# Performance work log

Measured on AMD Instinct MI355X. Metric: run time of the kernel, lower is better.

The kernel has to match this reference:

```python
import jax, jax.numpy as jnp
import numpy as np

TOP_K = 2


def setup_inputs() -> dict:
    key = jax.random.key(0)
    k1, k2, k3, k4, k5 = jax.random.split(key, 5)
    B, S, D, E, F = 2, 1024, 2048, 8, 768
    scale_in = 1.0 / np.sqrt(D)
    scale_ff = 1.0 / np.sqrt(F)
    return {
        "x": jax.random.normal(k1, (B, S, D), dtype=jnp.float32),
        "w_gate_router": jax.random.normal(k2, (E, D), dtype=jnp.float32) * scale_in,
        "w_gate_proj": jax.random.normal(k3, (E, F, D), dtype=jnp.float32) * scale_in,
        "w_up_proj": jax.random.normal(k4, (E, F, D), dtype=jnp.float32) * scale_in,
        "w_down_proj": jax.random.normal(k5, (E, D, F), dtype=jnp.float32) * scale_ff,
    }


def moe_forward(x, w_gate_router, w_gate_proj, w_up_proj, w_down_proj):
    E = w_gate_router.shape[0]
    # Router: scores [B,S,E], top-k selection, softmax over the k selected scores.
    scores = jnp.einsum("bsd,ed->bse", x, w_gate_router)
    topk_scores, topk_idx = jax.lax.top_k(scores, TOP_K)          # [B,S,K]
    topk_probs = jax.nn.softmax(topk_scores, axis=-1)             # [B,S,K]
    # Dense combine weights: zero for unselected experts (== scatter of topk_probs).
    weights = jnp.sum(topk_probs[..., None] * jax.nn.one_hot(topk_idx, E, dtype=x.dtype), axis=-2)  # [B,S,E]
    # Per-expert SwiGLU computed densely over all tokens (same math as
    # gather/dispatch-per-expert followed by scatter-add combine).
    gate = jnp.einsum("bsd,efd->bsef", x, w_gate_proj)            # [B,S,E,F]
    up = jnp.einsum("bsd,efd->bsef", x, w_up_proj)
    hidden = jax.nn.silu(gate) * up                                # [B,S,E,F]
    # Weighted combine: sum_e weights[b,s,e] * (hidden @ w_down[e].T)
    out = jnp.einsum("bsef,edf,bse->bsd", hidden, w_down_proj, weights)
    return out


def reference(x, w_gate_router, w_gate_proj, w_up_proj, w_down_proj):
    return moe_forward(x, w_gate_router, w_gate_proj, w_up_proj, w_down_proj)
```

## Files before the change

### kernel.cpp

```cpp
#include <hip/hip_runtime.h>

#define T_TOK 2048
#define DIM   2048
#define NEXP  8
#define FF    768
#define NGRP  16
#define BK    64

typedef unsigned short u16;
typedef unsigned int   u32;
typedef __bf16 bf16x8 __attribute__((ext_vector_type(8)));
typedef float  f32x4  __attribute__((ext_vector_type(4)));
typedef u16    u16x4  __attribute__((ext_vector_type(4)));
typedef u16    u16x8  __attribute__((ext_vector_type(8)));

#define AS1 __attribute__((address_space(1)))
#define AS3 __attribute__((address_space(3)))

__device__ __forceinline__ u16 f2bf(float f) {
    union { u32 i; float f; } v; v.f = f;
    u32 r = v.i + 0x7FFF + ((v.i >> 16) & 1);
    return (u16)(r >> 16);
}
__device__ __forceinline__ float bf2f(u16 u) {
    union { u32 i; float f; } v; v.i = ((u32)u) << 16; return v.f;
}

__device__ __forceinline__ void gload16(const u16* g, u16* l) {
    __builtin_amdgcn_global_load_lds((const AS1 u32*)g, (AS3 u32*)l, 16, 0, 0);
}

__global__ void cvt3_kernel(const float* __restrict__ s0, u16* __restrict__ d0,
                            const float* __restrict__ s1, u16* __restrict__ d1,
                            const float* __restrict__ s2, u16* __restrict__ d2) {
    const float* __restrict__ s; u16* __restrict__ d;
    switch (blockIdx.y) {
        case 0: s = s0; d = d0; break;
        case 1: s = s1; d = d1; break;
        default: s = s2; d = d2; break;
    }
    const size_t st = 1536u * 256u;
    size_t t = (size_t)blockIdx.x * 256 + threadIdx.x;
#pragma unroll
    for (int it = 0; it < 4; it++) {
        size_t i = t + (size_t)it * st;
        f32x4 a = ((const f32x4*)s)[i * 2];
        f32x4 b = ((const f32x4*)s)[i * 2 + 1];
        u16x8 o;
#pragma unroll
        for (int j = 0; j < 4; j++) { o[j] = f2bf(a[j]); o[4 + j] = f2bf(b[j]); }
        ((u16x8*)d)[i] = o;
    }
}

__global__ void router_kernel(const float* __restrict__ x, const float* __restrict__ wr,
                              int* cnt, int* rt_e, float* rt_p, u16* __restrict__ xb) {
    int wave = threadIdx.x >> 6, lane = threadIdx.x & 63;
    int t = blockIdx.x * 4 + wave;
    float xv[32];
#pragma unroll
    for (int i = 0; i < 32; i++) xv[i] = x[(size_t)t * DIM + i * 64 + lane];
#pragma unroll
    for (int i = 0; i < 32; i++) xb[(size_t)t * DIM + i * 64 + lane] = f2bf(xv[i]);
    float s[NEXP];
#pragma unroll
    for (int e = 0; e < NEXP; e++) {
        float acc = 0.f;
#pragma unroll
        for (int i = 0; i < 32; i++) acc += xv[i] * wr[(size_t)e * DIM + i * 64 + lane];
        for (int off = 32; off; off >>= 1) acc += __shfl_xor(acc, off);
        s[e] = acc;
    }
    if (lane == 0) {
        int bi = 0; float bv = s[0];
        for (int e = 1; e < NEXP; e++) if (s[e] > bv) { bv = s[e]; bi = e; }
        float sv = -1e30f; int si = 0;
        for (int e = 0; e < NEXP; e++) { if (e == bi) continue; if (s[e] > sv) { sv = s[e]; si = e; } }
        float p0 = 1.f / (1.f + __expf(sv - bv));
        float p1 = 1.f - p0;
        rt_e[t * 2 + 0] = bi; rt_e[t * 2 + 1] = si;
        rt_p[t * 2 + 0] = p0; rt_p[t * 2 + 1] = p1;
        atomicAdd(&cnt[bi * 2 + 0], 1);
        atomicAdd(&cnt[si * 2 + 1], 1);
    }
}

__global__ void scanassign_kernel(const int* cnt, const int* rt_e, const float* rt_p,
                                  int* base_g, int* tile_g, int* tile_m0, int* ntiles,
                                  int* rowtok, float* rowprob) {
    __shared__ int s_base[NGRP];
    __shared__ int s_pos[NGRP];
    int tid = threadIdx.x;
    if (tid < NGRP) s_pos[tid] = 0;
    if (tid < 64) {
        int lane = tid;
        int c = (lane < NGRP) ? cnt[lane] : 0;
        int nt_g = (c + 127) >> 7;
        int pre = 0, tpre = 0;
        for (int i = 0; i < NGRP; i++) {
            int ci = __shfl(c, i), ti = __shfl(nt_g, i);
            if (i < lane) { pre += ci; tpre += ti; }
        }
        if (lane < NGRP) {
            s_base[lane] = pre; base_g[lane] = pre;
            for (int j = 0; j < nt_g; j++) { tile_g[tpre + j] = lane; tile_m0[tpre + j] = j * 128; }
            if (lane == NGRP - 1) *ntiles = tpre + nt_g;
        }
    }
    __syncthreads();
    for (int t = tid; t < T_TOK; t += 256) {
#pragma unroll
        for (int k = 0; k < 2; k++) {
            int g = rt_e[t * 2 + k] * 2 + k;
            int pos = atomicAdd(&s_pos[g], 1);
            int row = s_base[g] + pos;
            rowtok[row] = t;
            rowprob[row] = rt_p[t * 2 + k];
        }
    }
}

__launch_bounds__(256)
__global__ void gateup_kernel(const u16* __restrict__ xb, const u16* __restrict__ wgb,
                              const u16* __restrict__ wub,
                              const int* cnt, const int* base, const int* tile_g,
                              const int* tile_m0, const int* ntiles,
                              const int* rowtok, const float* rowprob,
                              u16* __restrict__ hidden) {
    int tile = blockIdx.x;
    if (tile >= *ntiles) return;
    int g = tile_g[tile], m0 = tile_m0[tile];
    int e = g >> 1;
    int f0 = blockIdx.y * 64;
    int cg = cnt[g], bg_ = base[g];

    __shared__ u16 As[2][128 * BK];
    __shared__ u16 Bs[2][128 * BK];
    __shared__ int   tks[128];
    __shared__ float ps[128];

    int tid = threadIdx.x;
    if (tid < 128) {
        int valid = (m0 + tid) < cg;
        tks[tid] = valid ? rowtok[bg_ + m0 + tid] : 0;
        ps[tid]  = valid ? rowprob[bg_ + m0 + tid] : 0.f;
    }
    __syncthreads();

    int wave = tid >> 6, lane = tid & 63;
    int quad = lane >> 4, l16 = lane & 15;
    int wr = wave >> 1, wc = wave & 1;

    int r8  = lane >> 3;
    int csw = ((lane & 7) ^ r8) * 8;

    const u16* gA[4]; int lA[4];
#pragma unroll
    for (int gi = 0; gi < 4; gi++) {
        int row = wave * 32 + gi * 8 + r8;
        gA[gi] = xb + (size_t)tks[row] * DIM + csw;
        lA[gi] = (wave * 32 + gi * 8) * BK;
    }
    const u16* bsrc = (wave >> 1) ? wub : wgb;
    int fo = (wave & 1) * 8 + r8;
    const u16* gB[4]; int lB[4];
#pragma unroll
    for (int gi = 0; gi < 4; gi++) {
        gB[gi] = bsrc + ((size_t)e * FF + f0 + gi * 16 + fo) * DIM + csw;
        lB[gi] = (gi * 32 + wave * 8) * BK;
    }

    f32x4 acc[4][4] = {};

#pragma unroll
    for (int gi = 0; gi < 4; gi++) gload16(gA[gi], &As[0][0] + lA[gi]);
#pragma unroll
    for (int gi = 0; gi < 4; gi++) gload16(gB[gi], &Bs[0][0] + lB[gi]);

    int sw0 = ((0 * 4 + quad) ^ (l16 & 7)) * 8;
    int sw1 = ((1 * 4 + quad) ^ (l16 & 7)) * 8;

    for (int kt = 0; kt < DIM / BK; kt++) {
        int cur = kt & 1;
        int kk = (kt + 1) * BK;
        if (kk < DIM) {
#pragma unroll
            for (int gi = 0; gi < 4; gi++) gload16(gA[gi] + kk, &As[cur ^ 1][0] + lA[gi]);
#pragma unroll
            for (int gi = 0; gi < 4; gi++) gload16(gB[gi] + kk, &Bs[cur ^ 1][0] + lB[gi]);
            __builtin_amdgcn_sched_barrier(0);
            asm volatile("s_waitcnt vmcnt(8)" ::: "memory");
        } else {
            __builtin_amdgcn_sched_barrier(0);
            asm volatile("s_waitcnt vmcnt(0)" ::: "memory");
        }
        __builtin_amdgcn_s_barrier();
        __builtin_amdgcn_sched_barrier(0);
#pragma unroll
        for (int ks = 0; ks < 2; ks++) {
            int sw = ks ? sw1 : sw0;
            bf16x8 a[4], b[4];
#pragma unroll
            for (int mi = 0; mi < 4; mi++)
                a[mi] = *(const bf16x8*)&As[cur][(wr * 64 + mi * 16 + l16) * BK + sw];
#pragma unroll
            for (int ni = 0; ni < 4; ni++)
                b[ni] = *(const bf16x8*)&Bs[cur][(wc * 64 + ni * 16 + l16) * BK + sw];
#pragma unroll
            for (int mi = 0; mi < 4; mi++)
#pragma unroll
                for (int ni = 0; ni < 4; ni++)
                    acc[mi][ni] = __builtin_amdgcn_mfma_f32_16x16x32_bf16(a[mi], b[ni], acc[mi][ni], 0, 0, 0);
        }
        __builtin_amdgcn_sched_barrier(0);
        asm volatile("s_waitcnt lgkmcnt(0)" ::: "memory");
        __builtin_amdgcn_s_barrier();
    }

    int fb = f0 + wc * 32 + l16;
#pragma unroll
    for (int mi = 0; mi < 4; mi++) {
#pragma unroll
        for (int r = 0; r < 4; r++) {
            int m = wr * 64 + mi * 16 + quad * 4 + r;
            if (m0 + m < cg) {
                float p = ps[m];
                float g0 = acc[mi][0][r], u0 = acc[mi][1][r];
                float g1 = acc[mi][2][r], u1 = acc[mi][3][r];
                size_t rowo = (size_t)(bg_ + m0 + m) * FF;
                hidden[rowo + fb]      = f2bf((g0 / (1.f + __expf(-g0))) * u0 * p);
                hidden[rowo + fb + 16] = f2bf((g1 / (1.f + __expf(-g1))) * u1 * p);
            }
        }
    }
}

__launch_bounds__(256)
__global__ void down_kernel(const u16* __restrict__ hid, const u16* __restrict__ wdb,
                            const int* cnt, const int* base, const int* tile_g,
                            const int* tile_m0, const int* ntiles, const int* rowtok,
                            u16* __restrict__ out0, u16* __restrict__ out1) {
    int tile = blockIdx.x;
    if (tile >= *ntiles) return;
    int g = tile_g[tile], m0 = tile_m0[tile];
    int e = g >> 1, slot = g & 1;
    int d0 = blockIdx.y * 128;
    int cg = cnt[g], bg_ = base[g];

    __shared__ u16 As[2][128 * BK];
    __shared__ u16 Bs[2][128 * BK];
    __shared__ int tks[128];

    int tid = threadIdx.x;
    if (tid < 128) tks[tid] = ((m0 + tid) < cg) ? rowtok[bg_ + m0 + tid] : 0;
    __syncthreads();

    int wave = tid >> 6, lane = tid & 63;
    int quad = lane >> 4, l16 = lane & 15;
    int wr = wave >> 1, wc = wave & 1;

    int r8  = lane >> 3;
    int csw = ((lane & 7) ^ r8) * 8;

    const u16* gA[4]; int lA[4];
#pragma unroll
    for (int gi = 0; gi < 4; gi++) {
        int row = wave * 32 + gi * 8 + r8;
        gA[gi] = hid + (size_t)(bg_ + m0 + row) * FF + csw;
        lA[gi] = (wave * 32 + gi * 8) * BK;
    }
    const u16* gB[4]; int lB[4];
#pragma unroll
    for (int gi = 0; gi < 4; gi++) {
        int n = gi * 32 + wave * 8 + r8;
        gB[gi] = wdb + ((size_t)e * DIM + d0 + n) * FF + csw;
        lB[gi] = (gi * 32 + wave * 8) * BK;
    }

    f32x4 acc[4][4] = {};

#pragma unroll
    for (int gi = 0; gi < 4; gi++) gload16(gA[gi], &As[0][0] + lA[gi]);
#pragma unroll
    for (int gi = 0; gi < 4; gi++) gload16(gB[gi], &Bs[0][0] + lB[gi]);

    int sw0 = ((0 * 4 + quad) ^ (l16 & 7)) * 8;
    int sw1 = ((1 * 4 + quad) ^ (l16 & 7)) * 8;

    for (int kt = 0; kt < FF / BK; kt++) {
        int cur = kt & 1;
        int kk = (kt + 1) * BK;
        if (kk < FF) {
#pragma unroll
            for (int gi = 0; gi < 4; gi++) gload16(gA[gi] + kk, &As[cur ^ 1][0] + lA[gi]);
#pragma unroll
            for (int gi = 0; gi < 4; gi++) gload16(gB[gi] + kk, &Bs[cur ^ 1][0] + lB[gi]);
            __builtin_amdgcn_sched_barrier(0);
            asm volatile("s_waitcnt vmcnt(8)" ::: "memory");
        } else {
            __builtin_amdgcn_sched_barrier(0);
            asm volatile("s_waitcnt vmcnt(0)" ::: "memory");
        }
        __builtin_amdgcn_s_barrier();
        __builtin_amdgcn_sched_barrier(0);
#pragma unroll
        for (int ks = 0; ks < 2; ks++) {
            int sw = ks ? sw1 : sw0;
            bf16x8 a[4], b[4];
#pragma unroll
            for (int mi = 0; mi < 4; mi++)
                a[mi] = *(const bf16x8*)&As[cur][(wr * 64 + mi * 16 + l16) * BK + sw];
#pragma unroll
            for (int ni = 0; ni < 4; ni++)
                b[ni] = *(const bf16x8*)&Bs[cur][(wc * 64 + ni * 16 + l16) * BK + sw];
#pragma unroll
            for (int mi = 0; mi < 4; mi++)
#pragma unroll
                for (int ni = 0; ni < 4; ni++)
                    acc[mi][ni] = __builtin_amdgcn_mfma_f32_16x16x32_bf16(a[mi], b[ni], acc[mi][ni], 0, 0, 0);
        }
        __builtin_amdgcn_sched_barrier(0);
        asm volatile("s_waitcnt lgkmcnt(0)" ::: "memory");
        __builtin_amdgcn_s_barrier();
    }

    u16* outp = slot ? out1 : out0;
#pragma unroll
    for (int mi = 0; mi < 4; mi++) {
#pragma unroll
        for (int ni = 0; ni < 4; ni++) {
            int d = d0 + wc * 64 + ni * 16 + l16;
#pragma unroll
            for (int r = 0; r < 4; r++) {
                int m = wr * 64 + mi * 16 + quad * 4 + r;
                if (m0 + m < cg) {
                    outp[(size_t)tks[m] * DIM + d] = f2bf(acc[mi][ni][r]);
                }
            }
        }
    }
}

__global__ void combine_kernel(const u16* __restrict__ o0, const u16* __restrict__ o1,
                               float* __restrict__ out) {
    int i = blockIdx.x * blockDim.x + threadIdx.x;
    u16x8 a = *(const u16x8*)(o0 + (size_t)i * 8);
    u16x8 b = *(const u16x8*)(o1 + (size_t)i * 8);
    f32x4 r0, r1;
#pragma unroll
    for (int j = 0; j < 4; j++) {
        r0[j] = bf2f(a[j]) + bf2f(b[j]);
        r1[j] = bf2f(a[4 + j]) + bf2f(b[4 + j]);
    }
    *(f32x4*)(out + (size_t)i * 8) = r0;
    *(f32x4*)(out + (size_t)i * 8 + 4) = r1;
}

extern "C" void kernel_launch(void* const* d_in, const int* in_sizes, int n_in,
                              void* d_out, int out_size, void* d_ws, size_t ws_size,
                              hipStream_t stream) {
    const float* x  = (const float*)d_in[0];
    const float* wr = (const float*)d_in[1];
    const float* wg = (const float*)d_in[2];
    const float* wu = (const float*)d_in[3];
    const float* wd = (const float*)d_in[4];
    float* out = (float*)d_out;

    char* W = (char*)d_ws;
    int*   cnt     = (int*)(W + 0);
    int*   base    = (int*)(W + 128);
    int*   ntiles  = (int*)(W + 192);
    int*   tile_g  = (int*)(W + 256);
    int*   tile_m0 = (int*)(W + 512);
    int*   rt_e    = (int*)(W + 1024);
    float* rt_p    = (float*)(W + 20480);
    int*   rowtok  = (int*)(W + 40960);
    float* rowprob = (float*)(W + 61440);
    u16*   hidden  = (u16*)(W + 81920);
    u16*   xb      = (u16*)(W + ((size_t)8  << 20));
    u16*   wgb     = (u16*)(W + ((size_t)17 << 20));
    u16*   wub     = (u16*)(W + ((size_t)43 << 20));
    u16*   wdb     = (u16*)(W + ((size_t)69 << 20));
    u16*   out0    = (u16*)(W + ((size_t)17 << 20));
    u16*   out1    = (u16*)(W + ((size_t)26 << 20));

    hipMemsetAsync(W, 0, 256, stream);

    cvt3_kernel<<<dim3(1536, 3), 256, 0, stream>>>(wg, wgb, wu, wub, wd, wdb);

    router_kernel<<<T_TOK / 4, 256, 0, stream>>>(x, wr, cnt, rt_e, rt_p, xb);
    scanassign_kernel<<<1, 256, 0, stream>>>(cnt, rt_e, rt_p, base, tile_g, tile_m0,
                                             ntiles, rowtok, rowprob);

    gateup_kernel<<<dim3(48, 12), 256, 0, stream>>>(xb, wgb, wub, cnt, base, tile_g, tile_m0,
                                                    ntiles, rowtok, rowprob, hidden);
    down_kernel<<<dim3(48, 16), 256, 0, stream>>>(hidden, wdb, cnt, base, tile_g, tile_m0,
                                                  ntiles, rowtok, out0, out1);
    combine_kernel<<<T_TOK * DIM / (256 * 8), 256, 0, stream>>>(out0, out1, out);
}
```

Measured before the change: 371.9 us.

## Shrink GEMM tiles to 128x64 with BK=32 to double block count

Both the gate/up and down grouped GEMM kernels move from 128x128 tiles with BK=64 to 128x64 tiles with BK=32. The global-to-LDS load mapping, swizzle pattern and wait counts are reworked to match, and the grid's y dimension is doubled. The aim is to launch more workgroups and lower per-block LDS and register use, giving better CU occupancy on a small, ragged MoE workload. In exchange, each MFMA has less data reuse, there are more barriers per unit of K, and A tiles are loaded twice as often.

```diff
diff --git a/kernel.cpp b/kernel.cpp
--- a/kernel.cpp
+++ b/kernel.cpp
@@ -5,7 +5,7 @@
 #define NEXP  8
 #define FF    768
 #define NGRP  16
-#define BK    64
+#define BK    32
 
 typedef unsigned short u16;
 typedef unsigned int   u32;
@@ -131,11 +131,11 @@
     if (tile >= *ntiles) return;
     int g = tile_g[tile], m0 = tile_m0[tile];
     int e = g >> 1;
-    int f0 = blockIdx.y * 64;
+    int f0 = blockIdx.y * 32;
     int cg = cnt[g], bg_ = base[g];
 
     __shared__ u16 As[2][128 * BK];
-    __shared__ u16 Bs[2][128 * BK];
+    __shared__ u16 Bs[2][64 * BK];
     __shared__ int   tks[128];
     __shared__ float ps[128];
 
@@ -151,85 +151,69 @@
     int quad = lane >> 4, l16 = lane & 15;
     int wr = wave >> 1, wc = wave & 1;
 
-    int r8  = lane >> 3;
-    int csw = ((lane & 7) ^ r8) * 8;
-
-    const u16* gA[4]; int lA[4];
-#pragma unroll
-    for (int gi = 0; gi < 4; gi++) {
-        int row = wave * 32 + gi * 8 + r8;
-        gA[gi] = xb + (size_t)tks[row] * DIM + csw;
-        lA[gi] = (wave * 32 + gi * 8) * BK;
-    }
-    const u16* bsrc = (wave >> 1) ? wub : wgb;
-    int fo = (wave & 1) * 8 + r8;
-    const u16* gB[4]; int lB[4];
-#pragma unroll
-    for (int gi = 0; gi < 4; gi++) {
-        gB[gi] = bsrc + ((size_t)e * FF + f0 + gi * 16 + fo) * DIM + csw;
-        lB[gi] = (gi * 32 + wave * 8) * BK;
-    }
-
-    f32x4 acc[4][4] = {};
-
-#pragma unroll
-    for (int gi = 0; gi < 4; gi++) gload16(gA[gi], &As[0][0] + lA[gi]);
-#pragma unroll
-    for (int gi = 0; gi < 4; gi++) gload16(gB[gi], &Bs[0][0] + lB[gi]);
-
-    int sw0 = ((0 * 4 + quad) ^ (l16 & 7)) * 8;
-    int sw1 = ((1 * 4 + quad) ^ (l16 & 7)) * 8;
+    int r4 = lane >> 2;
+    int cw = ((lane & 3) ^ ((r4 >> 1) & 3)) * 8;
+
+    const u16* gA0 = xb + (size_t)tks[wave * 32 + r4] * DIM + cw;
+    const u16* gA1 = xb + (size_t)tks[wave * 32 + 16 + r4] * DIM + cw;
+    int lA0 = (wave * 32) * BK, lA1 = (wave * 32 + 16) * BK;
+    const u16* bsrc = (wave & 1) ? wub : wgb;
+    const u16* gB = bsrc + ((size_t)e * FF + f0 + (wave >> 1) * 16 + r4) * DIM + cw;
+    int lB = (wave * 16) * BK;
+
+    int swz = (quad ^ ((l16 >> 1) & 3)) * 8;
+    int aoff[4], boff[2];
+#pragma unroll
+    for (int mi = 0; mi < 4; mi++) aoff[mi] = (wr * 64 + mi * 16 + l16) * BK + swz;
+#pragma unroll
+    for (int ni = 0; ni < 2; ni++) boff[ni] = (wc * 32 + ni * 16 + l16) * BK + swz;
+
+    f32x4 acc[4][2] = {};
+
+    gload16(gA0, &As[0][0] + lA0);
+    gload16(gA1, &As[0][0] + lA1);
+    gload16(gB,  &Bs[0][0] + lB);
 
     for (int kt = 0; kt < DIM / BK; kt++) {
         int cur = kt & 1;
         int kk = (kt + 1) * BK;
         if (kk < DIM) {
-#pragma unroll
-            for (int gi = 0; gi < 4; gi++) gload16(gA[gi] + kk, &As[cur ^ 1][0] + lA[gi]);
-#pragma unroll
-            for (int gi = 0; gi < 4; gi++) gload16(gB[gi] + kk, &Bs[cur ^ 1][0] + lB[gi]);
+            gload16(gA0 + kk, &As[cur ^ 1][0] + lA0);
+            gload16(gA1 + kk, &As[cur ^ 1][0] + lA1);
+            gload16(gB + kk,  &Bs[cur ^ 1][0] + lB);
             __builtin_amdgcn_sched_barrier(0);
-            asm volatile("s_waitcnt vmcnt(8)" ::: "memory");
+            asm volatile("s_waitcnt vmcnt(3)" ::: "memory");
         } else {
             __builtin_amdgcn_sched_barrier(0);
             asm volatile("s_waitcnt vmcnt(0)" ::: "memory");
         }
         __builtin_amdgcn_s_barrier();
         __builtin_amdgcn_sched_barrier(0);
-#pragma unroll
-        for (int ks = 0; ks < 2; ks++) {
-            int sw = ks ? sw1 : sw0;
-            bf16x8 a[4], b[4];
-#pragma unroll
-            for (int mi = 0; mi < 4; mi++)
-                a[mi] = *(const bf16x8*)&As[cur][(wr * 64 + mi * 16 + l16) * BK + sw];
-#pragma unroll
-            for (int ni = 0; ni < 4; ni++)
-                b[ni] = *(const bf16x8*)&Bs[cur][(wc * 64 + ni * 16 + l16) * BK + sw];
-#pragma unroll
-            for (int mi = 0; mi < 4; mi++)
-#pragma unroll
-                for (int ni = 0; ni < 4; ni++)
-                    acc[mi][ni] = __builtin_amdgcn_mfma_f32_16x16x32_bf16(a[mi], b[ni], acc[mi][ni], 0, 0, 0);
-        }
+        bf16x8 a[4], b[2];
+#pragma unroll
+        for (int mi = 0; mi < 4; mi++) a[mi] = *(const bf16x8*)&As[cur][aoff[mi]];
+#pragma unroll
+        for (int ni = 0; ni < 2; ni++) b[ni] = *(const bf16x8*)&Bs[cur][boff[ni]];
+#pragma unroll
+        for (int mi = 0; mi < 4; mi++)
+#pragma unroll
+            for (int ni = 0; ni < 2; ni++)
+                acc[mi][ni] = __builtin_amdgcn_mfma_f32_16x16x32_bf16(a[mi], b[ni], acc[mi][ni], 0, 0, 0);
         __builtin_amdgcn_sched_barrier(0);
         asm volatile("s_waitcnt lgkmcnt(0)" ::: "memory");
         __builtin_amdgcn_s_barrier();
     }
 
-    int fb = f0 + wc * 32 + l16;
+    int f = f0 + wc * 16 + l16;
 #pragma unroll
     for (int mi = 0; mi < 4; mi++) {
 #pragma unroll
         for (int r = 0; r < 4; r++) {
             int m = wr * 64 + mi * 16 + quad * 4 + r;
             if (m0 + m < cg) {
-                float p = ps[m];
-                float g0 = acc[mi][0][r], u0 = acc[mi][1][r];
-                float g1 = acc[mi][2][r], u1 = acc[mi][3][r];
-                size_t rowo = (size_t)(bg_ + m0 + m) * FF;
-                hidden[rowo + fb]      = f2bf((g0 / (1.f + __expf(-g0))) * u0 * p);
-                hidden[rowo + fb + 16] = f2bf((g1 / (1.f + __expf(-g1))) * u1 * p);
+                float gv = acc[mi][0][r], uv = acc[mi][1][r];
+                float h = (gv / (1.f + __expf(-gv))) * uv * ps[m];
+                hidden[(size_t)(bg_ + m0 + m) * FF + f] = f2bf(h);
             }
         }
     }
@@ -244,11 +228,11 @@
     if (tile >= *ntiles) return;
     int g = tile_g[tile], m0 = tile_m0[tile];
     int e = g >> 1, slot = g & 1;
-    int d0 = blockIdx.y * 128;
+    int d0 = blockIdx.y * 64;
     int cg = cnt[g], bg_ = base[g];
 
     __shared__ u16 As[2][128 * BK];
-    __shared__ u16 Bs[2][128 * BK];
+    __shared__ u16 Bs[2][64 * BK];
     __shared__ int tks[128];
 
     int tid = threadIdx.x;
@@ -259,66 +243,53 @@
     int quad = lane >> 4, l16 = lane & 15;
     int wr = wave >> 1, wc = wave & 1;
 
-    int r8  = lane >> 3;
-    int csw = ((lane & 7) ^ r8) * 8;
-
-    const u16* gA[4]; int lA[4];
-#pragma unroll
-    for (int gi = 0; gi < 4; gi++) {
-        int row = wave * 32 + gi * 8 + r8;
-        gA[gi] = hid + (size_t)(bg_ + m0 + row) * FF + csw;
-        lA[gi] = (wave * 32 + gi * 8) * BK;
-    }
-    const u16* gB[4]; int lB[4];
-#pragma unroll
-    for (int gi = 0; gi < 4; gi++) {
-        int n = gi * 32 + wave * 8 + r8;
-        gB[gi] = wdb + ((size_t)e * DIM + d0 + n) * FF + csw;
-        lB[gi] = (gi * 32 + wave * 8) * BK;
-    }
-
-    f32x4 acc[4][4] = {};
-
-#pragma unroll
-    for (int gi = 0; gi < 4; gi++) gload16(gA[gi], &As[0][0] + lA[gi]);
-#pragma unroll
-    for (int gi = 0; gi < 4; gi++) gload16(gB[gi], &Bs[0][0] + lB[gi]);
-
-    int sw0 = ((0 * 4 + quad) ^ (l16 & 7)) * 8;
-    int sw1 = ((1 * 4 + quad) ^ (l16 & 7)) * 8;
+    int r4 = lane >> 2;
+    int cw = ((lane & 3) ^ ((r4 >> 1) & 3)) * 8;
+
+    const u16* gA0 = hid + (size_t)(bg_ + m0 + wave * 32 + r4) * FF + cw;
+    const u16* gA1 = hid + (size_t)(bg_ + m0 + wave * 32 + 16 + r4) * FF + cw;
+    int lA0 = (wave * 32) * BK, lA1 = (wave * 32 + 16) * BK;
+    const u16* gB = wdb + ((size_t)e * DIM + d0 + wave * 16 + r4) * FF + cw;
+    int lB = (wave * 16) * BK;
+
+    int swz = (quad ^ ((l16 >> 1) & 3)) * 8;
+    int aoff[4], boff[2];
+#pragma unroll
+    for (int mi = 0; mi < 4; mi++) aoff[mi] = (wr * 64 + mi * 16 + l16) * BK + swz;
+#pragma unroll
+    for (int ni = 0; ni < 2; ni++) boff[ni] = (wc * 32 + ni * 16 + l16) * BK + swz;
+
+    f32x4 acc[4][2] = {};
+
+    gload16(gA0, &As[0][0] + lA0);
+    gload16(gA1, &As[0][0] + lA1);
+    gload16(gB,  &Bs[0][0] + lB);
 
     for (int kt = 0; kt < FF / BK; kt++) {
         int cur = kt & 1;
         int kk = (kt + 1) * BK;
         if (kk < FF) {
-#pragma unroll
-            for (int gi = 0; gi < 4; gi++) gload16(gA[gi] + kk, &As[cur ^ 1][0] + lA[gi]);
-#pragma unroll
-            for (int gi = 0; gi < 4; gi++) gload16(gB[gi] + kk, &Bs[cur ^ 1][0] + lB[gi]);
+            gload16(gA0 + kk, &As[cur ^ 1][0] + lA0);
+            gload16(gA1 + kk, &As[cur ^ 1][0] + lA1);
+            gload16(gB + kk,  &Bs[cur ^ 1][0] + lB);
             __builtin_amdgcn_sched_barrier(0);
-            asm volatile("s_waitcnt vmcnt(8)" ::: "memory");
+            asm volatile("s_waitcnt vmcnt(3)" ::: "memory");
         } else {
             __builtin_amdgcn_sched_barrier(0);
             asm volatile("s_waitcnt vmcnt(0)" ::: "memory");
         }
         __builtin_amdgcn_s_barrier();
         __builtin_amdgcn_sched_barrier(0);
-#pragma unroll
-        for (int ks = 0; ks < 2; ks++) {
-            int sw = ks ? sw1 : sw0;
-            bf16x8 a[4], b[4];
-#pragma unroll
-            for (int mi = 0; mi < 4; mi++)
-                a[mi] = *(const bf16x8*)&As[cur][(wr * 64 + mi * 16 + l16) * BK + sw];
-#pragma unroll
-            for (int ni = 0; ni < 4; ni++)
-                b[ni] = *(const bf16x8*)&Bs[cur][(wc * 64 + ni * 16 + l16) * BK + sw];
-#pragma unroll
-            for (int mi = 0; mi < 4; mi++)
-#pragma unroll
-                for (int ni = 0; ni < 4; ni++)
-                    acc[mi][ni] = __builtin_amdgcn_mfma_f32_16x16x32_bf16(a[mi], b[ni], acc[mi][ni], 0, 0, 0);
-        }
+        bf16x8 a[4], b[2];
+#pragma unroll
+        for (int mi = 0; mi < 4; mi++) a[mi] = *(const bf16x8*)&As[cur][aoff[mi]];
+#pragma unroll
+        for (int ni = 0; ni < 2; ni++) b[ni] = *(const bf16x8*)&Bs[cur][boff[ni]];
+#pragma unroll
+        for (int mi = 0; mi < 4; mi++)
+#pragma unroll
+            for (int ni = 0; ni < 2; ni++)
+                acc[mi][ni] = __builtin_amdgcn_mfma_f32_16x16x32_bf16(a[mi], b[ni], acc[mi][ni], 0, 0, 0);
         __builtin_amdgcn_sched_barrier(0);
         asm volatile("s_waitcnt lgkmcnt(0)" ::: "memory");
         __builtin_amdgcn_s_barrier();
@@ -328,8 +299,8 @@
 #pragma unroll
     for (int mi = 0; mi < 4; mi++) {
 #pragma unroll
-        for (int ni = 0; ni < 4; ni++) {
-            int d = d0 + wc * 64 + ni * 16 + l16;
+        for (int ni = 0; ni < 2; ni++) {
+            int d = d0 + wc * 32 + ni * 16 + l16;
 #pragma unroll
             for (int r = 0; r < 4; r++) {
                 int m = wr * 64 + mi * 16 + quad * 4 + r;
@@ -392,9 +363,9 @@
     scanassign_kernel<<<1, 256, 0, stream>>>(cnt, rt_e, rt_p, base, tile_g, tile_m0,
                                              ntiles, rowtok, rowprob);
 
-    gateup_kernel<<<dim3(48, 12), 256, 0, stream>>>(xb, wgb, wub, cnt, base, tile_g, tile_m0,
+    gateup_kernel<<<dim3(48, 24), 256, 0, stream>>>(xb, wgb, wub, cnt, base, tile_g, tile_m0,
                                                     ntiles, rowtok, rowprob, hidden);
-    down_kernel<<<dim3(48, 16), 256, 0, stream>>>(hidden, wdb, cnt, base, tile_g, tile_m0,
+    down_kernel<<<dim3(48, 32), 256, 0, stream>>>(hidden, wdb, cnt, base, tile_g, tile_m0,
                                                   ntiles, rowtok, out0, out1);
     combine_kernel<<<T_TOK * DIM / (256 * 8), 256, 0, stream>>>(out0, out1, out);
 }
```

New measurement: 381.2 us. +2.5%, slower.
